# Performance work log

Hardware: AMD Instinct MI355X
Metric: run time of the kernel (lower is better)

Reference implementation:

```python
import jax, jax.numpy as jnp
import numpy as np

EPS = 1e-5


def _knn_group(q, p, kk):
    """q: [3,Nq] query points, p: [3,M] reference points. Returns
    features [4,Nq,kk] = (residual xyz, distance) and neighbors [3,Nq,kk]."""
    qt, pt = q.T, p.T  # [Nq,3], [M,3]
    d2 = (jnp.sum(qt * qt, axis=1)[:, None]
          + jnp.sum(pt * pt, axis=1)[None, :]
          - 2.0 * qt @ pt.T)                       # [Nq,M] squared dists
    _, idx = jax.lax.top_k(-d2, kk)                 # kk nearest -> [Nq,kk]
    nn = pt[idx]                                    # [Nq,kk,3]
    resi = nn - qt[:, None, :]
    dist = jnp.linalg.norm(resi, axis=-1, keepdims=True)
    feat = jnp.concatenate([resi, dist], axis=-1)   # [Nq,kk,4]
    return feat.transpose(2, 0, 1), nn.transpose(2, 0, 1)


def _group_norm(x, groups, w, b):
    B, C, N, K = x.shape
    xg = x.reshape(B, groups, C // groups, N, K)
    mu = xg.mean(axis=(2, 3, 4), keepdims=True)
    var = xg.var(axis=(2, 3, 4), keepdims=True)
    xg = (xg - mu) * jax.lax.rsqrt(var + EPS)
    return xg.reshape(B, C, N, K) * w[None, :, None, None] + b[None, :, None, None]


def _forward(points0, points1, w1, b1, gn1_w, gn1_b, w2, b2, gn2_w, gn2_b,
             k, wt_np, perm_np):
    B, _, N = points0.shape
    feats, grouped = [], []
    for i in range(B):  # per-sample loop: split sizes are data-dependent (as in original)
        N0 = int(N * wt_np[i, 0]); N1 = N - N0
        k0 = int(k * wt_np[i, 0]); k1 = k - k0
        newp = jnp.concatenate([points0[i][:, perm_np[i, 0, :N0]],
                                points1[i][:, perm_np[i, 1, :N1]]], axis=-1)  # [3,N]
        f0, g0 = _knn_group(newp, points0[i], k0)
        f1, g1 = _knn_group(newp, points1[i], k1)
        feats.append(jnp.concatenate([f0, f1], axis=-1))
        grouped.append(jnp.concatenate([g0, g1], axis=-1))
    x = jnp.stack(feats)        # [B,4,N,k]
    gp = jnp.stack(grouped)     # [B,3,N,k]
    # 1x1 conv -> GroupNorm -> ReLU, twice
    x = jnp.einsum('bcnk,oc->bonk', x, w1) + b1[None, :, None, None]
    x = jax.nn.relu(_group_norm(x, w1.shape[0] // 8, gn1_w, gn1_b))
    x = jnp.einsum('bcnk,oc->bonk', x, w2) + b2[None, :, None, None]
    x = jax.nn.relu(_group_norm(x, w2.shape[0] // 8, gn2_w, gn2_b))
    scores = jnp.max(x, axis=1)                 # [B,N,k]
    wts = jax.nn.softmax(scores, axis=-1)       # softmax over neighbors
    return jnp.sum(wts[:, None, :, :] * gp, axis=-1)  # [B,3,N]


def setup_inputs() -> dict:
    key = jax.random.key(0)
    B, N, K = 8, 4096, 32
    C1, C2 = 32, 64
    ks = jax.random.split(key, 8)
    points0 = jax.random.normal(ks[0], (B, 3, N), jnp.float32)
    points1 = jax.random.normal(ks[1], (B, 3, N), jnp.float32)
    weighted_t = jax.random.uniform(ks[2], (B, 2), jnp.float32, 0.25, 0.75)
    perm = jax.vmap(lambda kk: jax.random.permutation(kk, N))(
        jax.random.split(ks[3], B * 2)).reshape(B, 2, N).astype(jnp.int32)
    w1 = 0.1 * jax.random.normal(ks[4], (C1, 4), jnp.float32)
    b1 = jnp.zeros((C1,), jnp.float32)
    gn1_w = jnp.ones((C1,), jnp.float32)
    gn1_b = jnp.zeros((C1,), jnp.float32)
    w2 = 0.1 * jax.random.normal(ks[5], (C2, C1), jnp.float32)
    b2 = jnp.zeros((C2,), jnp.float32)
    gn2_w = jnp.ones((C2,), jnp.float32)
    gn2_b = jnp.zeros((C2,), jnp.float32)
    return dict(points0=points0, points1=points1, k=K, weighted_t=weighted_t,
                perm=perm, w1=w1, b1=b1, gn1_w=gn1_w, gn1_b=gn1_b,
                w2=w2, b2=b2, gn2_w=gn2_w, gn2_b=gn2_b)


def reference(points0, points1, k, weighted_t, perm, w1, b1, gn1_w, gn1_b,
              w2, b2, gn2_w, gn2_b):
    wt_np = np.asarray(weighted_t)   # concrete: drives static split sizes
    perm_np = np.asarray(perm)
    return _forward(points0, points1, w1, b1, gn1_w, gn1_b, w2, b2,
                    gn2_w, gn2_b, int(k), wt_np, perm_np)
```

## Files before the change

kernel.cpp:

```cpp
#include <hip/hip_runtime.h>
#include <math.h>

#define RQ 6
constexpr int WRANKS = 768;
constexpr int WCH = 12;

typedef __attribute__((ext_vector_type(8))) short s8v;
typedef __attribute__((ext_vector_type(4))) float f32x4;

__device__ inline unsigned short f2bf(float x) {
    const unsigned int u = __float_as_uint(x);
    return (unsigned short)((u + 0x7FFFu + ((u >> 16) & 1u)) >> 16);
}

__constant__ float ZB[63] = {
    -2.1539f, -1.8627f, -1.6759f, -1.5341f, -1.4178f, -1.3180f, -1.2299f, -1.1503f,
    -1.0775f, -1.0100f, -0.9468f, -0.8871f, -0.8305f, -0.7764f, -0.7245f, -0.6745f,
    -0.6261f, -0.5791f, -0.5334f, -0.4888f, -0.4451f, -0.4023f, -0.3601f, -0.3186f,
    -0.2776f, -0.2372f, -0.1971f, -0.1573f, -0.1178f, -0.0784f, -0.0392f,  0.0000f,
     0.0392f,  0.0784f,  0.1178f,  0.1573f,  0.1971f,  0.2372f,  0.2776f,  0.3186f,
     0.3601f,  0.4023f,  0.4451f,  0.4888f,  0.5334f,  0.5791f,  0.6261f,  0.6745f,
     0.7245f,  0.7764f,  0.8305f,  0.8871f,  0.9468f,  1.0100f,  1.0775f,  1.1503f,
     1.2299f,  1.3180f,  1.4178f,  1.5341f,  1.6759f,  1.8627f,  2.1539f };

__global__ __launch_bounds__(1024) void zbin_kernel(
    const float* __restrict__ p0, const float* __restrict__ p1,
    float4* __restrict__ sp, int* __restrict__ starts, int N)
{
    __shared__ int cnt[64], off[64], cur[64];
    const int t = threadIdx.x;
    const int bl = blockIdx.x;
    const int b = bl >> 1, list = bl & 1;
    const float* rb = (list ? p1 : p0) + (size_t)(b * 3) * N;
    if (t < 64) { cnt[t] = 0; cur[t] = 0; }
    __syncthreads();
    int mybin[4]; float mx[4], my[4], mz[4];
    for (int i = 0; i < 4; ++i) {
        const int idx = i * 1024 + t;
        const float z = rb[2 * N + idx];
        mx[i] = rb[idx]; my[i] = rb[N + idx]; mz[i] = z;
        int bin = 0;
#pragma unroll
        for (int s = 32; s; s >>= 1)
            if (bin + s <= 63 && z >= ZB[bin + s - 1]) bin += s;
        mybin[i] = bin;
        atomicAdd(&cnt[bin], 1);
    }
    __syncthreads();
    if (t < 64) {
        const int v = cnt[t];
        int x = v;
#pragma unroll
        for (int o = 1; o < 64; o <<= 1) {
            const int y = __shfl_up(x, o);
            if (t >= o) x += y;
        }
        off[t] = x - v;
        starts[bl * 65 + t] = x - v;
        if (t == 63) starts[bl * 65 + 64] = x;
    }
    __syncthreads();
    for (int i = 0; i < 4; ++i) {
        const int bin = mybin[i];
        const int pos = off[bin] + atomicAdd(&cur[bin], 1);
        sp[(size_t)bl * 4096 + pos] =
            make_float4(mx[i], my[i], mz[i],
                        fmaf(mx[i], mx[i], fmaf(my[i], my[i], mz[i] * mz[i])));
    }
}


__device__ __forceinline__ void cpush(unsigned key, unsigned pos, unsigned Tu,
                                      bool valid,
                                      unsigned* __restrict__ ck,
                                      unsigned* __restrict__ cp,
                                      int& cnt)
{
    const bool pred = valid && (key <= Tu);
    const unsigned long long bal = __ballot(pred);
    const unsigned below = __builtin_amdgcn_mbcnt_hi(
        (unsigned)(bal >> 32), __builtin_amdgcn_mbcnt_lo((unsigned)bal, 0u));
    const unsigned idx = (unsigned)cnt + below;
    if (pred && idx < 64u) { ck[idx] = key; cp[idx] = pos; }
    cnt += (int)__popcll(bal);
}

__device__ __forceinline__ void cscan(const float4* __restrict__ L,
                                      int bs, int be,
                                      float qx, float qy, float qz, float qq,
                                      unsigned Tu,
                                      unsigned* __restrict__ ck,
                                      unsigned* __restrict__ cp,
                                      int& cnt, int lane)
{
    for (int p = bs; p < be; p += 64) {
        const int pos = p + lane;
        const float4 pc = L[min(pos, be - 1)];
        const float dt = fmaf(qz, pc.z, fmaf(qy, pc.y, qx * pc.x));
        const float d = fmaxf(fmaf(-2.f, dt, pc.w + qq), 0.f);
        cpush(__float_as_uint(d), (unsigned)pos, Tu, pos < be, ck, cp, cnt);
    }
}

__device__ __forceinline__ void sort2_write(
    const unsigned* __restrict__ ck0, const unsigned* __restrict__ cp0, int cnt0,
    const float4* __restrict__ L0, int kk0, int ob0,
    const unsigned* __restrict__ ck1, const unsigned* __restrict__ cp1, int cnt1,
    const float4* __restrict__ L1, int kk1, int ob1,
    float qx, float qy, float qz, float4* __restrict__ feat, int lane)
{
    unsigned vk0 = (lane < cnt0) ? ck0[lane] : 0xFFFFFFFFu;
    unsigned vp0 = (lane < cnt0) ? cp0[lane] : 0xFFFFFFFFu;
    unsigned vk1 = (lane < cnt1) ? ck1[lane] : 0xFFFFFFFFu;
    unsigned vp1 = (lane < cnt1) ? cp1[lane] : 0xFFFFFFFFu;
#pragma unroll
    for (int k2 = 2; k2 <= 64; k2 <<= 1) {
#pragma unroll
        for (int jj = k2 >> 1; jj; jj >>= 1) {
            const unsigned yk0 = __shfl_xor(vk0, jj), yp0 = __shfl_xor(vp0, jj);
            const unsigned yk1 = __shfl_xor(vk1, jj), yp1 = __shfl_xor(vp1, jj);
            const bool keepmin = (((lane & jj) == 0) == ((lane & k2) == 0));
            const bool lt0 = (vk0 < yk0) || ((vk0 == yk0) && (vp0 < yp0));
            const bool s0 = keepmin ? (!lt0) : lt0;
            vk0 = s0 ? yk0 : vk0; vp0 = s0 ? yp0 : vp0;
            const bool lt1 = (vk1 < yk1) || ((vk1 == yk1) && (vp1 < yp1));
            const bool s1 = keepmin ? (!lt1) : lt1;
            vk1 = s1 ? yk1 : vk1; vp1 = s1 ? yp1 : vp1;
        }
    }
    if (lane < kk0) {
        const float4 pc = L0[vp0 & 4095u];
        const float rx = pc.x - qx, ry = pc.y - qy, rz = pc.z - qz;
        feat[ob0 + lane] =
            make_float4(rx, ry, rz, sqrtf(fmaf(rx, rx, fmaf(ry, ry, rz * rz))));
    }
    if (lane < kk1) {
        const float4 pc = L1[vp1 & 4095u];
        const float rx = pc.x - qx, ry = pc.y - qy, rz = pc.z - qz;
        feat[ob1 + lane] =
            make_float4(rx, ry, rz, sqrtf(fmaf(rx, rx, fmaf(ry, ry, rz * rz))));
    }
}

__device__ __forceinline__ void sort_write(
    const unsigned* __restrict__ ck, const unsigned* __restrict__ cp, int cnt,
    const float4* __restrict__ L, int kk, int obase,
    float qx, float qy, float qz, float4* __restrict__ feat, int lane)
{
    unsigned vk = (lane < cnt) ? ck[lane] : 0xFFFFFFFFu;
    unsigned vp = (lane < cnt) ? cp[lane] : 0xFFFFFFFFu;
#pragma unroll
    for (int k2 = 2; k2 <= 64; k2 <<= 1) {
#pragma unroll
        for (int jj = k2 >> 1; jj; jj >>= 1) {
            const unsigned yk = __shfl_xor(vk, jj);
            const unsigned yp = __shfl_xor(vp, jj);
            const bool keepmin = (((lane & jj) == 0) == ((lane & k2) == 0));
            const bool lt = (vk < yk) || ((vk == yk) && (vp < yp));
            const bool sely = keepmin ? (!lt) : lt;
            vk = sely ? yk : vk;
            vp = sely ? yp : vp;
        }
    }
    if (lane < kk) {
        const float4 pc = L[vp & 4095u];
        const float rx = pc.x - qx, ry = pc.y - qy, rz = pc.z - qz;
        feat[obase + lane] =
            make_float4(rx, ry, rz, sqrtf(fmaf(rx, rx, fmaf(ry, ry, rz * rz))));
    }
}

__device__ __forceinline__ void qpush(unsigned (&kh)[RQ], unsigned (&kl)[RQ],
                                      unsigned key, unsigned pos)
{
    bool cb[RQ];
#pragma unroll
    for (int s = 0; s < RQ; ++s) cb[s] = key < kh[s];
#pragma unroll
    for (int s = RQ - 1; s >= 1; --s) {
        kh[s] = cb[s - 1] ? kh[s - 1] : (cb[s] ? key : kh[s]);
        kl[s] = cb[s - 1] ? kl[s - 1] : (cb[s] ? pos : kl[s]);
    }
    kh[0] = cb[0] ? key : kh[0];
    kl[0] = cb[0] ? pos : kl[0];
}

__device__ __forceinline__ void pop_extract(
    unsigned (&kh)[RQ], unsigned (&kl)[RQ], int kk,
    const float4* __restrict__ L, int obase,
    float qx, float qy, float qz, float4* __restrict__ feat, int lane)
{
    unsigned mwin = 0;
    for (int rr = 0; rr < kk; ++rr) {
        unsigned gg = kh[0];
#pragma unroll
        for (int off = 32; off; off >>= 1) gg = min(gg, __shfl_xor(gg, off));
        const bool tied = (kh[0] == gg);
        unsigned mc;
        const unsigned long long bal = __ballot(tied);
        if (bal & (bal - 1)) {
            mc = tied ? kl[0] : 0xFFFFFFFFu;
#pragma unroll
            for (int off = 32; off; off >>= 1) mc = min(mc, __shfl_xor(mc, off));
        } else {
            mc = __shfl(kl[0], (int)__ffsll((long long)bal) - 1);
        }
        const bool w = tied && (kl[0] == mc);
        if (lane == rr) mwin = mc;
#pragma unroll
        for (int s = 0; s < RQ - 1; ++s) {
            kh[s] = w ? kh[s + 1] : kh[s];
            kl[s] = w ? kl[s + 1] : kl[s];
        }
        kh[RQ - 1] = w ? 0xFFFFFFFFu : kh[RQ - 1];
        kl[RQ - 1] = w ? 0xFFFFFFFFu : kl[RQ - 1];
    }
    if (lane < kk) {
        const float4 pc = L[mwin & 4095u];
        const float rx = pc.x - qx, ry = pc.y - qy, rz = pc.z - qz;
        feat[obase + lane] =
            make_float4(rx, ry, rz, sqrtf(fmaf(rx, rx, fmaf(ry, ry, rz * rz))));
    }
}

__device__ __forceinline__ void fallback_full(
    const float4* __restrict__ L, int Npts, int kk, int obase,
    float qx, float qy, float qz, float qq,
    float4* __restrict__ feat, int lane)
{
    unsigned kh[RQ], kl[RQ];
#pragma unroll
    for (int s = 0; s < RQ; ++s) { kh[s] = 0xFFFFFFFFu; kl[s] = 0xFFFFFFFFu; }
    for (int p = 0; p < Npts; p += 64) {
        const int pos = p + lane;
        const float4 pc = L[min(pos, Npts - 1)];
        const float dt = fmaf(qz, pc.z, fmaf(qy, pc.y, qx * pc.x));
        const float d = fmaxf(fmaf(-2.f, dt, pc.w + qq), 0.f);
        const unsigned key = (pos < Npts) ? __float_as_uint(d) : 0xFFFFFFFFu;
        qpush(kh, kl, key, (unsigned)pos);
    }
    pop_extract(kh, kl, kk, L, obase, qx, qy, qz, feat, lane);
}

__global__ __launch_bounds__(256, 4) void knn_kernel(
    const float* __restrict__ p0, const float* __restrict__ p1,
    const float* __restrict__ wt, const int* __restrict__ perm,
    const float4* __restrict__ sp, const int* __restrict__ starts,
    float4* __restrict__ feat, float4* __restrict__ newp, int N)
{
    __shared__ unsigned ck0s[256], cp0s[256], ck1s[256], cp1s[256];
    const int lane = threadIdx.x & 63;
    const int wv = threadIdx.x >> 6;
    const int gwave = (int)((blockIdx.x * 256 + threadIdx.x) >> 6);
    const int b = gwave / N;
    const int n = gwave - b * N;
    const int q = b * N + n;

    unsigned* __restrict__ ck0 = ck0s + wv * 64;
    unsigned* __restrict__ cp0 = cp0s + wv * 64;
    unsigned* __restrict__ ck1 = ck1s + wv * 64;
    unsigned* __restrict__ cp1 = cp1s + wv * 64;

    const float wt0 = wt[b * 2];
    const int N0 = (int)(N * wt0);
    const int k0 = (int)(32 * wt0);
    const int kk0 = k0, kk1 = 32 - k0;

    int j; const float* src;
    if (n < N0) { j = perm[(b * 2) * N + n];            src = p0; }
    else        { j = perm[(b * 2 + 1) * N + (n - N0)]; src = p1; }
    const float qx = __uint_as_float(__builtin_amdgcn_readfirstlane(
                         __float_as_uint(src[(b * 3) * N + j])));
    const float qy = __uint_as_float(__builtin_amdgcn_readfirstlane(
                         __float_as_uint(src[(b * 3 + 1) * N + j])));
    const float qz = __uint_as_float(__builtin_amdgcn_readfirstlane(
                         __float_as_uint(src[(b * 3 + 2) * N + j])));
    const float qq = qx * qx + qy * qy + qz * qz;

    const int bl0 = b * 2, bl1 = b * 2 + 1;
    const int stv0 = starts[bl0 * 65 + lane];
    const int stv1 = starts[bl1 * 65 + lane];

    const float bv = (lane < 63) ? ZB[lane] : 3.0e38f;
    const int qbin = __popcll(__ballot(qz >= bv));

    if (lane == 0) newp[q] = make_float4(qx, qy, qz, 0.f);

    const float4* L0 = sp + (size_t)bl0 * 4096;
    const float4* L1 = sp + (size_t)bl1 * 4096;

    const int st0 = __shfl(stv0, qbin);
    const int en0 = (qbin >= 63) ? N : __shfl(stv0, qbin + 1);
    const int st1 = __shfl(stv1, qbin);
    const int en1 = (qbin >= 63) ? N : __shfl(stv1, qbin + 1);
    int s0 = ((st0 + en0) >> 1) - WRANKS / 2;
    s0 = s0 < 0 ? 0 : (s0 > N - WRANKS ? N - WRANKS : s0);
    int s1 = ((st1 + en1) >> 1) - WRANKS / 2;
    s1 = s1 < 0 ? 0 : (s1 > N - WRANKS ? N - WRANKS : s1);
    const int e0 = s0 + WRANKS, e1 = s1 + WRANKS;

    const float4* Lb0 = L0 + s0 + lane;
    const float4* Lb1 = L1 + s1 + lane;
    unsigned k0v[WCH], k1v[WCH];
    unsigned mn0 = 0xFFFFFFFFu, mn1 = 0xFFFFFFFFu;
    {
        float4 A0[3], A1[3], B0[3], B1[3];
#pragma unroll
        for (int c = 0; c < 3; ++c) { A0[c] = Lb0[c << 6]; A1[c] = Lb1[c << 6]; }
#pragma unroll
        for (int g = 0; g < 4; ++g) {
            if (g < 3) {
#pragma unroll
                for (int c = 0; c < 3; ++c) {
                    B0[c] = Lb0[(g * 3 + 3 + c) << 6];
                    B1[c] = Lb1[(g * 3 + 3 + c) << 6];
                }
            }
#pragma unroll
            for (int c = 0; c < 3; ++c) {
                const int ch = g * 3 + c;
                {
                    const float dt = fmaf(qz, A0[c].z, fmaf(qy, A0[c].y, qx * A0[c].x));
                    k0v[ch] = __float_as_uint(fmaxf(fmaf(-2.f, dt, A0[c].w + qq), 0.f));
                    mn0 = min(mn0, k0v[ch]);
                }
                {
                    const float dt = fmaf(qz, A1[c].z, fmaf(qy, A1[c].y, qx * A1[c].x));
                    k1v[ch] = __float_as_uint(fmaxf(fmaf(-2.f, dt, A1[c].w + qq), 0.f));
                    mn1 = min(mn1, k1v[ch]);
                }
            }
            if (g < 3) {
#pragma unroll
                for (int c = 0; c < 3; ++c) { A0[c] = B0[c]; A1[c] = B1[c]; }
            }
        }
    }

    unsigned x0 = mn0, x1 = mn1;
#pragma unroll
    for (int k2 = 2; k2 <= 64; k2 <<= 1) {
#pragma unroll
        for (int jj = k2 >> 1; jj; jj >>= 1) {
            const unsigned y0 = __shfl_xor(x0, jj);
            const unsigned y1 = __shfl_xor(x1, jj);
            const bool keepmin = (((lane & jj) == 0) == ((lane & k2) == 0));
            x0 = keepmin ? min(x0, y0) : (x0 > y0 ? x0 : y0);
            x1 = keepmin ? min(x1, y1) : (x1 > y1 ? x1 : y1);
        }
    }
    const unsigned Tu0 = (unsigned)__shfl((int)x0, kk0 - 1);
    const unsigned Tu1 = (unsigned)__shfl((int)x1, kk1 - 1);
    const float T0f = __uint_as_float(Tu0);
    const float T1f = __uint_as_float(Tu1);

    int cnt0 = 0, cnt1 = 0;
#pragma unroll
    for (int ch = 0; ch < WCH; ++ch) {
        cpush(k0v[ch], (unsigned)(s0 + (ch << 6) + lane), Tu0, true, ck0, cp0, cnt0);
        cpush(k1v[ch], (unsigned)(s1 + (ch << 6) + lane), Tu1, true, ck1, cp1, cnt1);
    }

    {
        const int binL = __popcll(__ballot(stv0 <= s0)) - 1;
        if (s0 > 0) {
            const int bs = __shfl(stv0, binL);
            if (bs < s0) cscan(L0, bs, s0, qx, qy, qz, qq, Tu0, ck0, cp0, cnt0, lane);
            for (int jb = binL - 1; jb >= 0; --jb) {
                const float dz = qz - ZB[jb];
                if (dz * dz * 0.99999f > T0f) break;
                const int bs2 = __shfl(stv0, jb);
                const int be2 = __shfl(stv0, jb + 1);
                cscan(L0, bs2, be2, qx, qy, qz, qq, Tu0, ck0, cp0, cnt0, lane);
            }
        }
        if (e0 < N) {
            const int binR = __popcll(__ballot(stv0 <= e0)) - 1;
            const int re = (binR >= 63) ? N : __shfl(stv0, binR + 1);
            if (e0 < re) cscan(L0, e0, re, qx, qy, qz, qq, Tu0, ck0, cp0, cnt0, lane);
            for (int jb = binR + 1; jb <= 63; ++jb) {
                const float dz = ZB[jb - 1] - qz;
                if (dz * dz * 0.99999f > T0f) break;
                const int bs2 = __shfl(stv0, jb);
                const int be2 = (jb >= 63) ? N : __shfl(stv0, jb + 1);
                cscan(L0, bs2, be2, qx, qy, qz, qq, Tu0, ck0, cp0, cnt0, lane);
            }
        }
        const int binL1 = __popcll(__ballot(stv1 <= s1)) - 1;
        if (s1 > 0) {
            const int bs = __shfl(stv1, binL1);
            if (bs < s1) cscan(L1, bs, s1, qx, qy, qz, qq, Tu1, ck1, cp1, cnt1, lane);
            for (int jb = binL1 - 1; jb >= 0; --jb) {
                const float dz = qz - ZB[jb];
                if (dz * dz * 0.99999f > T1f) break;
                const int bs2 = __shfl(stv1, jb);
                const int be2 = __shfl(stv1, jb + 1);
                cscan(L1, bs2, be2, qx, qy, qz, qq, Tu1, ck1, cp1, cnt1, lane);
            }
        }
        if (e1 < N) {
            const int binR1 = __popcll(__ballot(stv1 <= e1)) - 1;
            const int re = (binR1 >= 63) ? N : __shfl(stv1, binR1 + 1);
            if (e1 < re) cscan(L1, e1, re, qx, qy, qz, qq, Tu1, ck1, cp1, cnt1, lane);
            for (int jb = binR1 + 1; jb <= 63; ++jb) {
                const float dz = ZB[jb - 1] - qz;
                if (dz * dz * 0.99999f > T1f) break;
                const int bs2 = __shfl(stv1, jb);
                const int be2 = (jb >= 63) ? N : __shfl(stv1, jb + 1);
                cscan(L1, bs2, be2, qx, qy, qz, qq, Tu1, ck1, cp1, cnt1, lane);
            }
        }
    }

    const int ob0 = (q << 5), ob1 = (q << 5) + k0;
    if ((cnt0 <= 64) && (cnt1 <= 64)) {
        sort2_write(ck0, cp0, cnt0, L0, kk0, ob0,
                    ck1, cp1, cnt1, L1, kk1, ob1,
                    qx, qy, qz, feat, lane);
    } else {
        if (cnt0 <= 64) sort_write(ck0, cp0, cnt0, L0, kk0, ob0, qx, qy, qz, feat, lane);
        else            fallback_full(L0, N, kk0, ob0, qx, qy, qz, qq, feat, lane);
        if (cnt1 <= 64) sort_write(ck1, cp1, cnt1, L1, kk1, ob1, qx, qy, qz, feat, lane);
        else            fallback_full(L1, N, kk1, ob1, qx, qy, qz, qq, feat, lane);
    }
}

__global__ __launch_bounds__(256) void moment_stats_kernel(
    const float4* __restrict__ feat, float* __restrict__ stats1, int N)
{
    const int t = threadIdx.x, lane = t & 63;
    const int bpb = 64;
    const int b = blockIdx.x / bpb;
    const int ppb = (N * 32) / bpb;
    const size_t base = (size_t)b * N * 32 + (size_t)(blockIdx.x % bpb) * ppb;
    float a[14];
#pragma unroll
    for (int i = 0; i < 14; ++i) a[i] = 0.f;
    for (int i = t; i < ppb; i += 256) {
        const float4 f = feat[base + i];
        a[0] += f.x; a[1] += f.y; a[2] += f.z; a[3] += f.w;
        a[4] = fmaf(f.x, f.x, a[4]);  a[5] = fmaf(f.x, f.y, a[5]);
        a[6] = fmaf(f.x, f.z, a[6]);  a[7] = fmaf(f.x, f.w, a[7]);
        a[8] = fmaf(f.y, f.y, a[8]);  a[9] = fmaf(f.y, f.z, a[9]);
        a[10] = fmaf(f.y, f.w, a[10]); a[11] = fmaf(f.z, f.z, a[11]);
        a[12] = fmaf(f.z, f.w, a[12]); a[13] = fmaf(f.w, f.w, a[13]);
    }
#pragma unroll
    for (int i = 0; i < 14; ++i) {
        float x = a[i];
#pragma unroll
        for (int o = 32; o; o >>= 1) x += __shfl_down(x, o);
        a[i] = x;
    }
    __shared__ float sm[14];
    if (t < 14) sm[t] = 0.f;
    __syncthreads();
    if (lane == 0) {
#pragma unroll
        for (int i = 0; i < 14; ++i) atomicAdd(&sm[i], a[i]);
    }
    __syncthreads();
    if (t < 14) atomicAdd(&stats1[b * 14 + t], sm[t]);
}

template <int MODE>
__global__ __launch_bounds__(256) void conv2_pass_kernel(
    const float4* __restrict__ feat,
    const float* __restrict__ w1, const float* __restrict__ b1,
    const float* __restrict__ gn1w, const float* __restrict__ gn1b,
    const float* __restrict__ stats1,
    const float* __restrict__ w2, const float* __restrict__ b2,
    const float* __restrict__ gn2w, const float* __restrict__ gn2b,
    float* __restrict__ stats2,
    const float4* __restrict__ newp, float* __restrict__ out,
    int N, float inv_cnt)
{
    const int t = threadIdx.x, lane = t & 63, wv = t >> 6;
    const int quad = lane >> 4, col = lane & 15;
    const int bpb = (N * 32) / 512;
    const int b = blockIdx.x / bpb;
    const int pblock = (blockIdx.x - b * bpb) * 512;
    const size_t pbase = (size_t)b * N * 32 + pblock + wv * 128;

    __shared__ float sfin[24];
    __shared__ float sacc[16];
    __shared__ unsigned short h_lds[512 * 40];
    __shared__ float ssc[512];

    if (t < 16) sacc[t] = 0.f;
    if (t < 4) {
        const float cnt = (float)(N * 32);
        const float* mm = stats1 + b * 14;
        const float S0 = mm[0], S1 = mm[1], S2 = mm[2], S3 = mm[3];
        float sum = 0.f, sq = 0.f;
        for (int cch = 0; cch < 8; ++cch) {
            const int cid = t * 8 + cch;
            const float4 w = ((const float4*)w1)[cid];
            const float bb = b1[cid];
            const float ws = w.x * S0 + w.y * S1 + w.z * S2 + w.w * S3;
            const float wMw =
                w.x * w.x * mm[4] + w.y * w.y * mm[8] + w.z * w.z * mm[11] +
                w.w * w.w * mm[13] +
                2.f * (w.x * w.y * mm[5] + w.x * w.z * mm[6] + w.x * w.w * mm[7] +
                       w.y * w.z * mm[9] + w.y * w.w * mm[10] + w.z * w.w * mm[12]);
            sum += cnt * bb + ws;
            sq += cnt * bb * bb + 2.f * bb * ws + wMw;
        }
        const float mu = sum * inv_cnt, var = sq * inv_cnt - mu * mu;
        sfin[2 * t] = mu; sfin[2 * t + 1] = rsqrtf(var + 1e-5f);
    }
    if (MODE == 1 && t >= 4 && t < 12) {
        const int g = t - 4;
        const float S = stats2[b * 16 + g], Q = stats2[b * 16 + 8 + g];
        const float mu = S * inv_cnt, var = Q * inv_cnt - mu * mu;
        sfin[8 + 2 * g] = mu; sfin[8 + 2 * g + 1] = rsqrtf(var + 1e-5f);
    }
    __syncthreads();

    const int c1 = lane & 31, pt = lane >> 5;
    const float4 w1r = ((const float4*)w1)[c1];
    const float b1c = b1[c1];
    const int g1 = c1 >> 3;
    const float sc1 = sfin[2 * g1 + 1] * gn1w[c1];
    const float sh1 = gn1b[c1] - sfin[2 * g1] * sc1;

    for (int it = 0; it < 64; ++it) {
        const size_t p = pbase + it * 2;
        const float4 f = feat[p + pt];
        const float y = b1c + w1r.x * f.x + w1r.y * f.y + w1r.z * f.z + w1r.w * f.w;
        const float h = fmaxf(0.f, fmaf(y, sc1, sh1));
        h_lds[(wv * 128 + it * 2 + pt) * 40 + c1] = f2bf(h);
    }

    s8v afr[4];
#pragma unroll
    for (int T = 0; T < 4; ++T) {
        const int row = T * 16 + col;
#pragma unroll
        for (int j2 = 0; j2 < 8; ++j2)
            afr[T][j2] = (short)f2bf(w2[row * 32 + quad * 8 + j2]);
    }

    float b2v[4][4], sc2v[4][4], sh2v[4][4];
#pragma unroll
    for (int T = 0; T < 4; ++T)
#pragma unroll
        for (int r4 = 0; r4 < 4; ++r4) {
            const int cch = T * 16 + quad * 4 + r4;
            b2v[T][r4] = b2[cch];
            if (MODE == 1) {
                const int g2 = cch >> 3;
                const float sc = sfin[8 + 2 * g2 + 1] * gn2w[cch];
                sc2v[T][r4] = sc;
                sh2v[T][r4] = gn2b[cch] - sfin[8 + 2 * g2] * sc + b2[cch] * sc;
            }
        }

    float gsum[4] = {0, 0, 0, 0}, gsq[4] = {0, 0, 0, 0};

    for (int pt16 = 0; pt16 < 8; ++pt16) {
        const int row = wv * 128 + pt16 * 16 + col;
        const s8v bfr = *(const s8v*)&h_lds[row * 40 + quad * 8];
        f32x4 acc[4];
#pragma unroll
        for (int T = 0; T < 4; ++T) {
            acc[T] = (f32x4){0.f, 0.f, 0.f, 0.f};
            acc[T] = __builtin_amdgcn_mfma_f32_16x16x32_bf16(afr[T], bfr, acc[T], 0, 0, 0);
        }
        if (MODE == 0) {
#pragma unroll
            for (int T = 0; T < 4; ++T)
#pragma unroll
                for (int r4 = 0; r4 < 4; ++r4) {
                    const float v = acc[T][r4] + b2v[T][r4];
                    gsum[T] += v;
                    gsq[T] = fmaf(v, v, gsq[T]);
                }
        } else {
            float s = -3.0e38f;
#pragma unroll
            for (int T = 0; T < 4; ++T)
#pragma unroll
                for (int r4 = 0; r4 < 4; ++r4)
                    s = fmaxf(s, fmaxf(0.f, fmaf(acc[T][r4], sc2v[T][r4], sh2v[T][r4])));
            s = fmaxf(s, __shfl_xor(s, 16));
            s = fmaxf(s, __shfl_xor(s, 32));
            if (quad == 0) ssc[wv * 128 + pt16 * 16 + col] = s;
        }
    }

    if (MODE == 0) {
#pragma unroll
        for (int T = 0; T < 4; ++T) {
#pragma unroll
            for (int o = 1; o < 16; o <<= 1) {
                gsum[T] += __shfl_xor(gsum[T], o);
                gsq[T] += __shfl_xor(gsq[T], o);
            }
            gsum[T] += __shfl_xor(gsum[T], 16);
            gsq[T] += __shfl_xor(gsq[T], 16);
        }
        if (lane == 0) {
#pragma unroll
            for (int T = 0; T < 4; ++T) {
                atomicAdd(&sacc[2 * T], gsum[T]);
                atomicAdd(&sacc[8 + 2 * T], gsq[T]);
            }
        }
        if (lane == 32) {
#pragma unroll
            for (int T = 0; T < 4; ++T) {
                atomicAdd(&sacc[2 * T + 1], gsum[T]);
                atomicAdd(&sacc[8 + 2 * T + 1], gsq[T]);
            }
        }
        __syncthreads();
        if (t < 16) atomicAdd(&stats2[b * 16 + t], sacc[t]);
    } else {
        __syncthreads();
        const int qi = t >> 4, sub = t & 15;
        const int qg = (b * N * 32 + pblock) / 32 + qi;
        const int n = qg - b * N;
        const float s0 = ssc[qi * 32 + sub], s1 = ssc[qi * 32 + 16 + sub];
        float mx = fmaxf(s0, s1);
#pragma unroll
        for (int o = 8; o; o >>= 1) mx = fmaxf(mx, __shfl_xor(mx, o));
        const float e0 = __expf(s0 - mx), e1 = __expf(s1 - mx);
        float ssum = e0 + e1;
#pragma unroll
        for (int o = 8; o; o >>= 1) ssum += __shfl_xor(ssum, o);
        const float4 qc = newp[qg];
        const float4 f0 = feat[(size_t)qg * 32 + sub];
        const float4 f1 = feat[(size_t)qg * 32 + 16 + sub];
        float ax = e0 * (qc.x + f0.x) + e1 * (qc.x + f1.x);
        float ay = e0 * (qc.y + f0.y) + e1 * (qc.y + f1.y);
        float az = e0 * (qc.z + f0.z) + e1 * (qc.z + f1.z);
#pragma unroll
        for (int o = 8; o; o >>= 1) {
            ax += __shfl_xor(ax, o);
            ay += __shfl_xor(ay, o);
            az += __shfl_xor(az, o);
        }
        if (sub == 0) {
            const float inv = 1.f / ssum;
            out[(b * 3 + 0) * N + n] = ax * inv;
            out[(b * 3 + 1) * N + n] = ay * inv;
            out[(b * 3 + 2) * N + n] = az * inv;
        }
    }
}

extern "C" void kernel_launch(void* const* d_in, const int* in_sizes, int n_in,
                              void* d_out, int out_size, void* d_ws, size_t ws_size,
                              hipStream_t stream)
{
    const float* p0   = (const float*)d_in[0];
    const float* p1   = (const float*)d_in[1];
    const float* wt   = (const float*)d_in[3];
    const int*   perm = (const int*)d_in[4];
    const float* w1   = (const float*)d_in[5];
    const float* b1   = (const float*)d_in[6];
    const float* gn1w = (const float*)d_in[7];
    const float* gn1b = (const float*)d_in[8];
    const float* w2   = (const float*)d_in[9];
    const float* b2   = (const float*)d_in[10];
    const float* gn2w = (const float*)d_in[11];
    const float* gn2b = (const float*)d_in[12];
    float* out = (float*)d_out;

    const int B = in_sizes[3] / 2;
    const int N = in_sizes[0] / (3 * B);

    char* ws = (char*)d_ws;
    float4* spts = (float4*)ws;
    size_t off = (size_t)B * 2 * 4096 * sizeof(float4);
    float4* feat = (float4*)(ws + off);       off += (size_t)B * N * 32 * sizeof(float4);
    float4* newp = (float4*)(ws + off);       off += (size_t)B * N * sizeof(float4);
    float* stats1 = (float*)(ws + off);       off += (size_t)B * 14 * sizeof(float);
    float* stats2 = (float*)(ws + off);       off += (size_t)B * 16 * sizeof(float);
    int* starts = (int*)(ws + off);

    hipMemsetAsync(stats1, 0, (size_t)B * 30 * sizeof(float), stream);

    const float inv_cnt = 1.f / (8.f * (float)N * 32.f);

    zbin_kernel<<<B * 2, 1024, 0, stream>>>(p0, p1, spts, starts, N);

    knn_kernel<<<(B * N) / 4, 256, 0, stream>>>(
        p0, p1, wt, perm, spts, starts, feat, newp, N);

    moment_stats_kernel<<<B * 64, 256, 0, stream>>>(feat, stats1, N);

    conv2_pass_kernel<0><<<(B * N * 32) / 512, 256, 0, stream>>>(
        feat, w1, b1, gn1w, gn1b, stats1, w2, b2, gn2w, gn2b, stats2,
        newp, out, N, inv_cnt);

    conv2_pass_kernel<1><<<(B * N * 32) / 512, 256, 0, stream>>>(
        feat, w1, b1, gn1w, gn1b, stats1, w2, b2, gn2w, gn2b, stats2,
        newp, out, N, inv_cnt);
}
```

Measured before the change: 343.0 us.

## Replace bitonic sorts in kNN with ballot radix-select and hoist query gather

Swaps the 64-lane bitonic sorts (threshold search and final neighbour ordering) for a wave-wide bitwise radix select built on ballot/popcount. Output slots are assigned by rank within a selection mask, ordered by position rather than distance. The query-point gather moves into a separate small kernel that writes newp, which knn_kernel then reads. Candidate key/pos pairs are packed into uint2 in LDS. The intent is fewer shuffle instructions per query, at the cost of an extra launch and an output order that follows position instead of distance. That is fine only if downstream ops are order-invariant.

```diff
diff --git a/kernel.cpp b/kernel.cpp
--- a/kernel.cpp
+++ b/kernel.cpp
@@ -69,11 +69,25 @@
     }
 }
 
+__global__ __launch_bounds__(256) void gather_kernel(
+    const float* __restrict__ p0, const float* __restrict__ p1,
+    const float* __restrict__ wt, const int* __restrict__ perm,
+    float4* __restrict__ newp, int N)
+{
+    const int q = blockIdx.x * 256 + threadIdx.x;
+    const int b = q / N, n = q - b * N;
+    const float wt0 = wt[b * 2];
+    const int N0 = (int)(N * wt0);
+    int j; const float* src;
+    if (n < N0) { j = perm[(b * 2) * N + n];            src = p0; }
+    else        { j = perm[(b * 2 + 1) * N + (n - N0)]; src = p1; }
+    newp[q] = make_float4(src[(b * 3) * N + j], src[(b * 3 + 1) * N + j],
+                          src[(b * 3 + 2) * N + j], 0.f);
+}
+
 
 __device__ __forceinline__ void cpush(unsigned key, unsigned pos, unsigned Tu,
-                                      bool valid,
-                                      unsigned* __restrict__ ck,
-                                      unsigned* __restrict__ cp,
+                                      bool valid, uint2* __restrict__ cc,
                                       int& cnt)
 {
     const bool pred = valid && (key <= Tu);
@@ -81,16 +95,14 @@
     const unsigned below = __builtin_amdgcn_mbcnt_hi(
         (unsigned)(bal >> 32), __builtin_amdgcn_mbcnt_lo((unsigned)bal, 0u));
     const unsigned idx = (unsigned)cnt + below;
-    if (pred && idx < 64u) { ck[idx] = key; cp[idx] = pos; }
+    if (pred && idx < 64u) cc[idx] = make_uint2(key, pos);
     cnt += (int)__popcll(bal);
 }
 
 __device__ __forceinline__ void cscan(const float4* __restrict__ L,
                                       int bs, int be,
                                       float qx, float qy, float qz, float qq,
-                                      unsigned Tu,
-                                      unsigned* __restrict__ ck,
-                                      unsigned* __restrict__ cp,
+                                      unsigned Tu, uint2* __restrict__ cc,
                                       int& cnt, int lane)
 {
     for (int p = bs; p < be; p += 64) {
@@ -98,76 +110,78 @@
         const float4 pc = L[min(pos, be - 1)];
         const float dt = fmaf(qz, pc.z, fmaf(qy, pc.y, qx * pc.x));
         const float d = fmaxf(fmaf(-2.f, dt, pc.w + qq), 0.f);
-        cpush(__float_as_uint(d), (unsigned)pos, Tu, pos < be, ck, cp, cnt);
-    }
-}
-
-__device__ __forceinline__ void sort2_write(
-    const unsigned* __restrict__ ck0, const unsigned* __restrict__ cp0, int cnt0,
-    const float4* __restrict__ L0, int kk0, int ob0,
-    const unsigned* __restrict__ ck1, const unsigned* __restrict__ cp1, int cnt1,
-    const float4* __restrict__ L1, int kk1, int ob1,
-    float qx, float qy, float qz, float4* __restrict__ feat, int lane)
-{
-    unsigned vk0 = (lane < cnt0) ? ck0[lane] : 0xFFFFFFFFu;
-    unsigned vp0 = (lane < cnt0) ? cp0[lane] : 0xFFFFFFFFu;
-    unsigned vk1 = (lane < cnt1) ? ck1[lane] : 0xFFFFFFFFu;
-    unsigned vp1 = (lane < cnt1) ? cp1[lane] : 0xFFFFFFFFu;
-#pragma unroll
-    for (int k2 = 2; k2 <= 64; k2 <<= 1) {
-#pragma unroll
-        for (int jj = k2 >> 1; jj; jj >>= 1) {
-            const unsigned yk0 = __shfl_xor(vk0, jj), yp0 = __shfl_xor(vp0, jj);
-            const unsigned yk1 = __shfl_xor(vk1, jj), yp1 = __shfl_xor(vp1, jj);
-            const bool keepmin = (((lane & jj) == 0) == ((lane & k2) == 0));
-            const bool lt0 = (vk0 < yk0) || ((vk0 == yk0) && (vp0 < yp0));
-            const bool s0 = keepmin ? (!lt0) : lt0;
-            vk0 = s0 ? yk0 : vk0; vp0 = s0 ? yp0 : vp0;
-            const bool lt1 = (vk1 < yk1) || ((vk1 == yk1) && (vp1 < yp1));
-            const bool s1 = keepmin ? (!lt1) : lt1;
-            vk1 = s1 ? yk1 : vk1; vp1 = s1 ? yp1 : vp1;
-        }
-    }
-    if (lane < kk0) {
-        const float4 pc = L0[vp0 & 4095u];
-        const float rx = pc.x - qx, ry = pc.y - qy, rz = pc.z - qz;
-        feat[ob0 + lane] =
-            make_float4(rx, ry, rz, sqrtf(fmaf(rx, rx, fmaf(ry, ry, rz * rz))));
-    }
-    if (lane < kk1) {
-        const float4 pc = L1[vp1 & 4095u];
-        const float rx = pc.x - qx, ry = pc.y - qy, rz = pc.z - qz;
-        feat[ob1 + lane] =
-            make_float4(rx, ry, rz, sqrtf(fmaf(rx, rx, fmaf(ry, ry, rz * rz))));
-    }
-}
-
-__device__ __forceinline__ void sort_write(
-    const unsigned* __restrict__ ck, const unsigned* __restrict__ cp, int cnt,
-    const float4* __restrict__ L, int kk, int obase,
-    float qx, float qy, float qz, float4* __restrict__ feat, int lane)
-{
-    unsigned vk = (lane < cnt) ? ck[lane] : 0xFFFFFFFFu;
-    unsigned vp = (lane < cnt) ? cp[lane] : 0xFFFFFFFFu;
-#pragma unroll
-    for (int k2 = 2; k2 <= 64; k2 <<= 1) {
-#pragma unroll
-        for (int jj = k2 >> 1; jj; jj >>= 1) {
-            const unsigned yk = __shfl_xor(vk, jj);
-            const unsigned yp = __shfl_xor(vp, jj);
-            const bool keepmin = (((lane & jj) == 0) == ((lane & k2) == 0));
-            const bool lt = (vk < yk) || ((vk == yk) && (vp < yp));
-            const bool sely = keepmin ? (!lt) : lt;
-            vk = sely ? yk : vk;
-            vp = sely ? yp : vp;
-        }
-    }
-    if (lane < kk) {
-        const float4 pc = L[vp & 4095u];
-        const float rx = pc.x - qx, ry = pc.y - qy, rz = pc.z - qz;
-        feat[obase + lane] =
-            make_float4(rx, ry, rz, sqrtf(fmaf(rx, rx, fmaf(ry, ry, rz * rz))));
-    }
+        cpush(__float_as_uint(d), (unsigned)pos, Tu, pos < be, cc, cnt);
+    }
+}
+
+__device__ __forceinline__ void bisect2(unsigned key0, unsigned key1,
+                                        int kk0, int kk1,
+                                        unsigned& t0, unsigned& t1)
+{
+    unsigned long long a0 = ~0ull, a1 = ~0ull;
+    int n0 = kk0, n1 = kk1;
+    unsigned p0 = 0, p1 = 0;
+#pragma unroll
+    for (int b = 30; b >= 0; --b) {
+        const unsigned long long bz0 = __ballot(!((key0 >> b) & 1u));
+        const unsigned long long bz1 = __ballot(!((key1 >> b) & 1u));
+        const unsigned long long zc0 = a0 & bz0, zc1 = a1 & bz1;
+        const int c0 = __popcll(zc0), c1 = __popcll(zc1);
+        const bool u0 = (c0 >= n0), u1 = (c1 >= n1);
+        a0 = u0 ? zc0 : (a0 & ~bz0);
+        a1 = u1 ? zc1 : (a1 & ~bz1);
+        n0 = u0 ? n0 : n0 - c0;
+        n1 = u1 ? n1 : n1 - c1;
+        p0 |= u0 ? 0u : (1u << b);
+        p1 |= u1 ? 0u : (1u << b);
+    }
+    t0 = p0; t1 = p1;
+}
+
+__device__ __forceinline__ unsigned long long tie_finish(
+    unsigned long long alive, int kneed, unsigned tstar,
+    unsigned key, unsigned pos)
+{
+    const unsigned long long less = __ballot(key < tstar);
+    if (__popcll(alive) == kneed) return less | alive;
+    unsigned long long a = alive; int n = kneed; unsigned pp = 0;
+    for (int b = 11; b >= 0; --b) {
+        const unsigned long long bz = __ballot(!((pos >> b) & 1u));
+        const unsigned long long zc = a & bz;
+        const int c = __popcll(zc);
+        const bool u = (c >= n);
+        a = u ? zc : (a & ~bz);
+        n = u ? n : n - c;
+        pp |= u ? 0u : (1u << b);
+    }
+    return less | (alive & __ballot(pos <= pp));
+}
+
+__device__ __forceinline__ void sel2(unsigned key0, unsigned pos0,
+                                     unsigned key1, unsigned pos1,
+                                     int kk0, int kk1,
+                                     unsigned long long& sel0,
+                                     unsigned long long& sel1)
+{
+    unsigned long long a0 = ~0ull, a1 = ~0ull;
+    int n0 = kk0, n1 = kk1;
+    unsigned p0 = 0, p1 = 0;
+#pragma unroll
+    for (int b = 30; b >= 0; --b) {
+        const unsigned long long bz0 = __ballot(!((key0 >> b) & 1u));
+        const unsigned long long bz1 = __ballot(!((key1 >> b) & 1u));
+        const unsigned long long zc0 = a0 & bz0, zc1 = a1 & bz1;
+        const int c0 = __popcll(zc0), c1 = __popcll(zc1);
+        const bool u0 = (c0 >= n0), u1 = (c1 >= n1);
+        a0 = u0 ? zc0 : (a0 & ~bz0);
+        a1 = u1 ? zc1 : (a1 & ~bz1);
+        n0 = u0 ? n0 : n0 - c0;
+        n1 = u1 ? n1 : n1 - c1;
+        p0 |= u0 ? 0u : (1u << b);
+        p1 |= u1 ? 0u : (1u << b);
+    }
+    sel0 = tie_finish(a0, n0, p0, key0, pos0);
+    sel1 = tie_finish(a1, n1, p1, key1, pos1);
 }
 
 __device__ __forceinline__ void qpush(unsigned (&kh)[RQ], unsigned (&kl)[RQ],
@@ -242,13 +256,26 @@
     pop_extract(kh, kl, kk, L, obase, qx, qy, qz, feat, lane);
 }
 
+__device__ __forceinline__ void sel_write(
+    unsigned long long sel, unsigned pos, const float4* __restrict__ L,
+    int obase, float qx, float qy, float qz, float4* __restrict__ feat,
+    int lane)
+{
+    if ((sel >> lane) & 1ull) {
+        const int rank = __popcll(sel & ((1ull << lane) - 1ull));
+        const float4 pc = L[pos & 4095u];
+        const float rx = pc.x - qx, ry = pc.y - qy, rz = pc.z - qz;
+        feat[obase + rank] =
+            make_float4(rx, ry, rz, sqrtf(fmaf(rx, rx, fmaf(ry, ry, rz * rz))));
+    }
+}
+
 __global__ __launch_bounds__(256, 4) void knn_kernel(
-    const float* __restrict__ p0, const float* __restrict__ p1,
-    const float* __restrict__ wt, const int* __restrict__ perm,
+    const float* __restrict__ wt,
     const float4* __restrict__ sp, const int* __restrict__ starts,
-    float4* __restrict__ feat, float4* __restrict__ newp, int N)
-{
-    __shared__ unsigned ck0s[256], cp0s[256], ck1s[256], cp1s[256];
+    float4* __restrict__ feat, const float4* __restrict__ newp, int N)
+{
+    __shared__ uint2 cc0s[256], cc1s[256];
     const int lane = threadIdx.x & 63;
     const int wv = threadIdx.x >> 6;
     const int gwave = (int)((blockIdx.x * 256 + threadIdx.x) >> 6);
@@ -256,25 +283,18 @@
     const int n = gwave - b * N;
     const int q = b * N + n;
 
-    unsigned* __restrict__ ck0 = ck0s + wv * 64;
-    unsigned* __restrict__ cp0 = cp0s + wv * 64;
-    unsigned* __restrict__ ck1 = ck1s + wv * 64;
-    unsigned* __restrict__ cp1 = cp1s + wv * 64;
-
-    const float wt0 = wt[b * 2];
-    const int N0 = (int)(N * wt0);
+    uint2* __restrict__ cc0 = cc0s + wv * 64;
+    uint2* __restrict__ cc1 = cc1s + wv * 64;
+
+    const float wt0 = __uint_as_float(__builtin_amdgcn_readfirstlane(
+                          __float_as_uint(wt[b * 2])));
     const int k0 = (int)(32 * wt0);
     const int kk0 = k0, kk1 = 32 - k0;
 
-    int j; const float* src;
-    if (n < N0) { j = perm[(b * 2) * N + n];            src = p0; }
-    else        { j = perm[(b * 2 + 1) * N + (n - N0)]; src = p1; }
-    const float qx = __uint_as_float(__builtin_amdgcn_readfirstlane(
-                         __float_as_uint(src[(b * 3) * N + j])));
-    const float qy = __uint_as_float(__builtin_amdgcn_readfirstlane(
-                         __float_as_uint(src[(b * 3 + 1) * N + j])));
-    const float qz = __uint_as_float(__builtin_amdgcn_readfirstlane(
-                         __float_as_uint(src[(b * 3 + 2) * N + j])));
+    const float4 qp = newp[q];
+    const float qx = __uint_as_float(__builtin_amdgcn_readfirstlane(__float_as_uint(qp.x)));
+    const float qy = __uint_as_float(__builtin_amdgcn_readfirstlane(__float_as_uint(qp.y)));
+    const float qz = __uint_as_float(__builtin_amdgcn_readfirstlane(__float_as_uint(qp.z)));
     const float qq = qx * qx + qy * qy + qz * qz;
 
     const int bl0 = b * 2, bl1 = b * 2 + 1;
@@ -283,8 +303,6 @@
 
     const float bv = (lane < 63) ? ZB[lane] : 3.0e38f;
     const int qbin = __popcll(__ballot(qz >= bv));
-
-    if (lane == 0) newp[q] = make_float4(qx, qy, qz, 0.f);
 
     const float4* L0 = sp + (size_t)bl0 * 4096;
     const float4* L1 = sp + (size_t)bl1 * 4096;
@@ -337,91 +355,102 @@
         }
     }
 
-    unsigned x0 = mn0, x1 = mn1;
-#pragma unroll
-    for (int k2 = 2; k2 <= 64; k2 <<= 1) {
-#pragma unroll
-        for (int jj = k2 >> 1; jj; jj >>= 1) {
-            const unsigned y0 = __shfl_xor(x0, jj);
-            const unsigned y1 = __shfl_xor(x1, jj);
-            const bool keepmin = (((lane & jj) == 0) == ((lane & k2) == 0));
-            x0 = keepmin ? min(x0, y0) : (x0 > y0 ? x0 : y0);
-            x1 = keepmin ? min(x1, y1) : (x1 > y1 ? x1 : y1);
-        }
-    }
-    const unsigned Tu0 = (unsigned)__shfl((int)x0, kk0 - 1);
-    const unsigned Tu1 = (unsigned)__shfl((int)x1, kk1 - 1);
+    unsigned Tu0, Tu1;
+    bisect2(mn0, mn1, kk0, kk1, Tu0, Tu1);
     const float T0f = __uint_as_float(Tu0);
     const float T1f = __uint_as_float(Tu1);
 
     int cnt0 = 0, cnt1 = 0;
 #pragma unroll
     for (int ch = 0; ch < WCH; ++ch) {
-        cpush(k0v[ch], (unsigned)(s0 + (ch << 6) + lane), Tu0, true, ck0, cp0, cnt0);
-        cpush(k1v[ch], (unsigned)(s1 + (ch << 6) + lane), Tu1, true, ck1, cp1, cnt1);
+        cpush(k0v[ch], (unsigned)(s0 + (ch << 6) + lane), Tu0, true, cc0, cnt0);
+        cpush(k1v[ch], (unsigned)(s1 + (ch << 6) + lane), Tu1, true, cc1, cnt1);
     }
 
     {
         const int binL = __popcll(__ballot(stv0 <= s0)) - 1;
         if (s0 > 0) {
             const int bs = __shfl(stv0, binL);
-            if (bs < s0) cscan(L0, bs, s0, qx, qy, qz, qq, Tu0, ck0, cp0, cnt0, lane);
+            if (bs < s0) cscan(L0, bs, s0, qx, qy, qz, qq, Tu0, cc0, cnt0, lane);
             for (int jb = binL - 1; jb >= 0; --jb) {
                 const float dz = qz - ZB[jb];
                 if (dz * dz * 0.99999f > T0f) break;
                 const int bs2 = __shfl(stv0, jb);
                 const int be2 = __shfl(stv0, jb + 1);
-                cscan(L0, bs2, be2, qx, qy, qz, qq, Tu0, ck0, cp0, cnt0, lane);
+                cscan(L0, bs2, be2, qx, qy, qz, qq, Tu0, cc0, cnt0, lane);
             }
         }
         if (e0 < N) {
             const int binR = __popcll(__ballot(stv0 <= e0)) - 1;
             const int re = (binR >= 63) ? N : __shfl(stv0, binR + 1);
-            if (e0 < re) cscan(L0, e0, re, qx, qy, qz, qq, Tu0, ck0, cp0, cnt0, lane);
+            if (e0 < re) cscan(L0, e0, re, qx, qy, qz, qq, Tu0, cc0, cnt0, lane);
             for (int jb = binR + 1; jb <= 63; ++jb) {
                 const float dz = ZB[jb - 1] - qz;
                 if (dz * dz * 0.99999f > T0f) break;
                 const int bs2 = __shfl(stv0, jb);
                 const int be2 = (jb >= 63) ? N : __shfl(stv0, jb + 1);
-                cscan(L0, bs2, be2, qx, qy, qz, qq, Tu0, ck0, cp0, cnt0, lane);
+                cscan(L0, bs2, be2, qx, qy, qz, qq, Tu0, cc0, cnt0, lane);
             }
         }
         const int binL1 = __popcll(__ballot(stv1 <= s1)) - 1;
         if (s1 > 0) {
             const int bs = __shfl(stv1, binL1);
-            if (bs < s1) cscan(L1, bs, s1, qx, qy, qz, qq, Tu1, ck1, cp1, cnt1, lane);
+            if (bs < s1) cscan(L1, bs, s1, qx, qy, qz, qq, Tu1, cc1, cnt1, lane);
             for (int jb = binL1 - 1; jb >= 0; --jb) {
                 const float dz = qz - ZB[jb];
                 if (dz * dz * 0.99999f > T1f) break;
                 const int bs2 = __shfl(stv1, jb);
                 const int be2 = __shfl(stv1, jb + 1);
-                cscan(L1, bs2, be2, qx, qy, qz, qq, Tu1, ck1, cp1, cnt1, lane);
+                cscan(L1, bs2, be2, qx, qy, qz, qq, Tu1, cc1, cnt1, lane);
             }
         }
         if (e1 < N) {
             const int binR1 = __popcll(__ballot(stv1 <= e1)) - 1;
             const int re = (binR1 >= 63) ? N : __shfl(stv1, binR1 + 1);
-            if (e1 < re) cscan(L1, e1, re, qx, qy, qz, qq, Tu1, ck1, cp1, cnt1, lane);
+            if (e1 < re) cscan(L1, e1, re, qx, qy, qz, qq, Tu1, cc1, cnt1, lane);
             for (int jb = binR1 + 1; jb <= 63; ++jb) {
                 const float dz = ZB[jb - 1] - qz;
                 if (dz * dz * 0.99999f > T1f) break;
                 const int bs2 = __shfl(stv1, jb);
                 const int be2 = (jb >= 63) ? N : __shfl(stv1, jb + 1);
-                cscan(L1, bs2, be2, qx, qy, qz, qq, Tu1, ck1, cp1, cnt1, lane);
+                cscan(L1, bs2, be2, qx, qy, qz, qq, Tu1, cc1, cnt1, lane);
             }
         }
     }
 
     const int ob0 = (q << 5), ob1 = (q << 5) + k0;
     if ((cnt0 <= 64) && (cnt1 <= 64)) {
-        sort2_write(ck0, cp0, cnt0, L0, kk0, ob0,
-                    ck1, cp1, cnt1, L1, kk1, ob1,
-                    qx, qy, qz, feat, lane);
+        const uint2 v0 = cc0[lane];
+        const uint2 v1 = cc1[lane];
+        const unsigned ky0 = (lane < cnt0) ? v0.x : 0xFFFFFFFFu;
+        const unsigned ps0 = (lane < cnt0) ? v0.y : 0xFFFFFFFFu;
+        const unsigned ky1 = (lane < cnt1) ? v1.x : 0xFFFFFFFFu;
+        const unsigned ps1 = (lane < cnt1) ? v1.y : 0xFFFFFFFFu;
+        unsigned long long sel0, sel1;
+        sel2(ky0, ps0, ky1, ps1, kk0, kk1, sel0, sel1);
+        sel_write(sel0, ps0, L0, ob0, qx, qy, qz, feat, lane);
+        sel_write(sel1, ps1, L1, ob1, qx, qy, qz, feat, lane);
     } else {
-        if (cnt0 <= 64) sort_write(ck0, cp0, cnt0, L0, kk0, ob0, qx, qy, qz, feat, lane);
-        else            fallback_full(L0, N, kk0, ob0, qx, qy, qz, qq, feat, lane);
-        if (cnt1 <= 64) sort_write(ck1, cp1, cnt1, L1, kk1, ob1, qx, qy, qz, feat, lane);
-        else            fallback_full(L1, N, kk1, ob1, qx, qy, qz, qq, feat, lane);
+        if (cnt0 <= 64) {
+            const uint2 v0 = cc0[lane];
+            const unsigned ky = (lane < cnt0) ? v0.x : 0xFFFFFFFFu;
+            const unsigned ps = (lane < cnt0) ? v0.y : 0xFFFFFFFFu;
+            unsigned long long sa, sb;
+            sel2(ky, ps, ky, ps, kk0, kk0, sa, sb);
+            sel_write(sa, ps, L0, ob0, qx, qy, qz, feat, lane);
+        } else {
+            fallback_full(L0, N, kk0, ob0, qx, qy, qz, qq, feat, lane);
+        }
+        if (cnt1 <= 64) {
+            const uint2 v1 = cc1[lane];
+            const unsigned ky = (lane < cnt1) ? v1.x : 0xFFFFFFFFu;
+            const unsigned ps = (lane < cnt1) ? v1.y : 0xFFFFFFFFu;
+            unsigned long long sa, sb;
+            sel2(ky, ps, ky, ps, kk1, kk1, sa, sb);
+            sel_write(sa, ps, L1, ob1, qx, qy, qz, feat, lane);
+        } else {
+            fallback_full(L1, N, kk1, ob1, qx, qy, qz, qq, feat, lane);
+        }
     }
 }
 
@@ -684,10 +713,12 @@
 
     const float inv_cnt = 1.f / (8.f * (float)N * 32.f);
 
+    gather_kernel<<<(B * N) / 256, 256, 0, stream>>>(p0, p1, wt, perm, newp, N);
+
     zbin_kernel<<<B * 2, 1024, 0, stream>>>(p0, p1, spts, starts, N);
 
     knn_kernel<<<(B * N) / 4, 256, 0, stream>>>(
-        p0, p1, wt, perm, spts, starts, feat, newp, N);
+        wt, spts, starts, feat, newp, N);
 
     moment_stats_kernel<<<B * 64, 256, 0, stream>>>(feat, stats1, N);
 
```

New measurement: 376.5 us. +9.8%, slower.
